# Performance work log

Hardware: AMD Instinct MI355X
Metric: run time of the kernel (lower is better)

Reference implementation:

```python
import jax, jax.numpy as jnp
import numpy as np

D_MODEL = 128
EXPAND = 8
D_INNER = EXPAND * D_MODEL            # 1024
HEADDIM = D_MODEL                     # headdim = int(in_channels*8/8)
NHEADS = D_INNER // HEADDIM           # 8
D_STATE = 128
D_CONV = 4
CONV_DIM = D_INNER + 2 * D_STATE      # 1280
D_IN_PROJ = 2 * D_INNER + 2 * D_STATE + NHEADS  # 2312
EPS = 1e-5
B_SZ, SEQ = 2, 2048


def setup_inputs() -> dict:
    key = jax.random.key(0)
    ks = jax.random.split(key, 16)
    n = jax.random.normal
    dt_init = jax.random.uniform(ks[4], (NHEADS,), minval=0.001, maxval=0.1)
    return dict(
        hidden_states=n(ks[0], (B_SZ, SEQ, D_MODEL), jnp.float32),
        w_in=n(ks[1], (D_IN_PROJ, D_MODEL), jnp.float32) / np.float32(np.sqrt(D_MODEL)),
        conv_w=n(ks[2], (CONV_DIM, D_CONV), jnp.float32) / np.float32(np.sqrt(D_CONV)),
        conv_b=n(ks[3], (CONV_DIM,), jnp.float32) * 0.01,
        dt_bias=jnp.log(jnp.expm1(dt_init)),  # inverse-softplus init (official)
        A_log=jnp.log(jax.random.uniform(ks[5], (NHEADS,), minval=1.0, maxval=16.0)),
        D_skip=jnp.ones((NHEADS,), jnp.float32),
        gnorm_w=jnp.ones((D_INNER,), jnp.float32),
        w_out=n(ks[6], (D_MODEL, D_INNER), jnp.float32) / np.float32(np.sqrt(D_INNER)),
        ln1_w=jnp.ones((D_MODEL,), jnp.float32),
        ln1_b=jnp.zeros((D_MODEL,), jnp.float32),
        ln2_w=jnp.ones((D_MODEL,), jnp.float32),
        ln2_b=jnp.zeros((D_MODEL,), jnp.float32),
        mlp_w=n(ks[7], (D_MODEL, D_MODEL), jnp.float32) / np.float32(np.sqrt(D_MODEL)),
        mlp_b=jnp.zeros((D_MODEL,), jnp.float32),
    )


def _layer_norm(x, w, b):
    m = x.mean(-1, keepdims=True)
    xc = x - m
    v = (xc * xc).mean(-1, keepdims=True)
    return xc * jax.lax.rsqrt(v + EPS) * w + b


def _mixer(u, w_in, conv_w, conv_b, dt_bias, A_log, D_skip, gnorm_w, w_out):
    b, l, _ = u.shape
    zxbcdt = u @ w_in.T                                    # (b,l,2312)
    z = zxbcdt[..., :D_INNER]                              # gate
    xBC = zxbcdt[..., D_INNER:D_INNER + CONV_DIM]
    dt = jax.nn.softplus(zxbcdt[..., -NHEADS:] + dt_bias)  # (b,l,h)
    # depthwise causal conv1d + SiLU
    xc = jnp.pad(xBC.swapaxes(1, 2), ((0, 0), (0, 0), (D_CONV - 1, 0)))
    xc = jax.lax.conv_general_dilated(xc, conv_w[:, None, :], (1,), 'VALID',
                                      feature_group_count=CONV_DIM)
    xBC = jax.nn.silu((xc + conv_b[None, :, None]).swapaxes(1, 2))
    x = xBC[..., :D_INNER].reshape(b, l, NHEADS, HEADDIM)  # (b,l,h,p)
    Bm = xBC[..., D_INNER:D_INNER + D_STATE]               # (b,l,n), ngroups=1
    Cm = xBC[..., D_INNER + D_STATE:]                      # (b,l,n)
    A = -jnp.exp(A_log)                                    # (h,)
    dA = jnp.exp(dt * A)                                   # (b,l,h)

    def step(S, inp):
        dA_t, dt_t, B_t, C_t, x_t = inp
        S = S * dA_t[:, :, None, None] + jnp.einsum('bh,bhp,bn->bhpn', dt_t, x_t, B_t)
        return S, jnp.einsum('bhpn,bn->bhp', S, C_t)

    S0 = jnp.zeros((b, NHEADS, HEADDIM, D_STATE), u.dtype)
    _, ys = jax.lax.scan(step, S0, (dA.swapaxes(0, 1), dt.swapaxes(0, 1),
                                    Bm.swapaxes(0, 1), Cm.swapaxes(0, 1),
                                    x.swapaxes(0, 1)))
    y = ys.swapaxes(0, 1) + D_skip[None, None, :, None] * x  # skip connection
    y = y.reshape(b, l, D_INNER) * jax.nn.silu(z)            # gated RMSNorm
    y = y * jax.lax.rsqrt((y * y).mean(-1, keepdims=True) + EPS) * gnorm_w
    return y @ w_out.T


def reference(hidden_states, w_in, conv_w, conv_b, dt_bias, A_log, D_skip,
              gnorm_w, w_out, ln1_w, ln1_b, ln2_w, ln2_b, mlp_w, mlp_b):
    residual = hidden_states
    h = _layer_norm(residual, ln1_w, ln1_b)
    h = _mixer(h, w_in, conv_w, conv_b, dt_bias, A_log, D_skip, gnorm_w, w_out)
    residual = h + residual
    h = _layer_norm(residual, ln2_w, ln2_b)
    return h @ mlp_w.T + mlp_b
```

## Files before the change

kernel.cpp:

```cpp
#include <hip/hip_runtime.h>
#include <hip/hip_bf16.h>

#define B_SZ 2
#define SEQ 2048
#define DMODEL 128
#define DINNER 1024
#define NHEADS 8
#define HEADDIM 128
#define DSTATE 128
#define CONVDIM 1280
#define NPROJ 2304
#define NTOK (B_SZ*SEQ)
#define CHUNK 64
#define NCHUNK (SEQ/CHUNK)
#define LDT 72

using bf16_t = __hip_bfloat16;
using short8 = __attribute__((ext_vector_type(8))) short;
using short4v= __attribute__((ext_vector_type(4))) short;
using f32x4  = __attribute__((ext_vector_type(4))) float;

__device__ __forceinline__ float silu_f(float x) { return x / (1.f + expf(-x)); }
__device__ __forceinline__ float bf2f(short s) {
    unsigned u = ((unsigned)(unsigned short)s) << 16;
    return __uint_as_float(u);
}
__device__ __forceinline__ short f2bf_s(float f) {
    bf16_t h = __float2bfloat16(f);
    return *(short*)&h;
}

__global__ __launch_bounds__(128) void head_fused(
        const float* __restrict__ hidden,
        const float* __restrict__ ln1_w, const float* __restrict__ ln1_b,
        const float* __restrict__ w_in,
        const float* __restrict__ dt_bias, const float* __restrict__ A_log,
        bf16_t* __restrict__ h_bf, float* __restrict__ dtb, float* __restrict__ ldAb,
        const float* __restrict__ wa, int na, const float* __restrict__ wb, int nb,
        const float* __restrict__ wc, int nc,
        bf16_t* __restrict__ oa, bf16_t* __restrict__ ob, bf16_t* __restrict__ oc) {
    int blk = blockIdx.x;
    if (blk >= NTOK) {
        int i = (blk - NTOK) * 128 + threadIdx.x;
        if (i < na) oa[i] = __float2bfloat16(wa[i]);
        else if (i < na + nb) ob[i - na] = __float2bfloat16(wb[i - na]);
        else if (i < na + nb + nc) oc[i - na - nb] = __float2bfloat16(wc[i - na - nb]);
        return;
    }
    int m = blk, t = threadIdx.x;
    int wave = t >> 6, lane = t & 63;
    __shared__ float sA[2], sB[2];
    __shared__ float sred[2][8];
    float v = hidden[(size_t)m*DMODEL + t];
    float s = v;
#pragma unroll
    for (int d = 1; d < 64; d <<= 1) s += __shfl_xor(s, d, 64);
    if (lane == 0) sA[wave] = s;
    __syncthreads();
    float mean = (sA[0] + sA[1]) * (1.f/128.f);
    float xc = v - mean;
    float q = xc * xc;
#pragma unroll
    for (int d = 1; d < 64; d <<= 1) q += __shfl_xor(q, d, 64);
    if (lane == 0) sB[wave] = q;
    __syncthreads();
    float var = (sB[0] + sB[1]) * (1.f/128.f);
    float o = xc * rsqrtf(var + 1e-5f) * ln1_w[t] + ln1_b[t];
    h_bf[(size_t)m*DMODEL + t] = __float2bfloat16(o);
#pragma unroll
    for (int hd = 0; hd < NHEADS; hd++) {
        float p = o * w_in[(size_t)(NPROJ + hd)*DMODEL + t];
#pragma unroll
        for (int d = 1; d < 64; d <<= 1) p += __shfl_xor(p, d, 64);
        if (lane == 0) sred[wave][hd] = p;
    }
    __syncthreads();
    if (t < NHEADS) {
        float ssum = sred[0][t] + sred[1][t] + dt_bias[t];
        float dtv = (ssum > 20.f) ? ssum : log1pf(expf(ssum));
        float Av = -expf(A_log[t]);
        dtb[m*NHEADS + t] = dtv;
        ldAb[m*NHEADS + t] = dtv * Av;
    }
}

__global__ __launch_bounds__(256) void gemm_bf(const bf16_t* __restrict__ A,
                                               const bf16_t* __restrict__ W,
                                               bf16_t* __restrict__ C,
                                               int M, int N, int K) {
    int tid = threadIdx.x;
    int wave = tid >> 6, lane = tid & 63;
    int m0 = blockIdx.x * 64 + wave * 16;
    int n0 = blockIdx.y * 64;
    int lr = lane & 15, quad = lane >> 4;
    f32x4 acc[4];
#pragma unroll
    for (int j = 0; j < 4; j++) acc[j] = (f32x4){0.f, 0.f, 0.f, 0.f};
    for (int k0 = 0; k0 < K; k0 += 32) {
        short8 a = *(const short8*)(A + (size_t)(m0 + lr)*K + k0 + quad*8);
#pragma unroll
        for (int j = 0; j < 4; j++) {
            short8 b = *(const short8*)(W + (size_t)(n0 + j*16 + lr)*K + k0 + quad*8);
            acc[j] = __builtin_amdgcn_mfma_f32_16x16x32_bf16(a, b, acc[j], 0, 0, 0);
        }
    }
#pragma unroll
    for (int j = 0; j < 4; j++)
#pragma unroll
        for (int r = 0; r < 4; r++) {
            int row = m0 + quad*4 + r;
            int col = n0 + j*16 + lr;
            C[(size_t)row*N + col] = __float2bfloat16(acc[j][r]);
        }
}

__global__ __launch_bounds__(256) void conv_silu(const bf16_t* __restrict__ zxb,
                                                 const float* __restrict__ conv_w,
                                                 const float* __restrict__ conv_b,
                                                 bf16_t* __restrict__ xBCb) {
    int idx = blockIdx.x * 256 + threadIdx.x;
    if (idx >= NTOK * CONVDIM / 4) return;
    int c4 = (idx % (CONVDIM/4)) * 4;
    int m  = idx / (CONVDIM/4);
    int b = m >> 11, l = m & (SEQ - 1);
    float acc[4];
    f32x4 wv[4];
#pragma unroll
    for (int j = 0; j < 4; j++) {
        acc[j] = conv_b[c4 + j];
        wv[j] = *(const f32x4*)(conv_w + (c4 + j)*4);
    }
#pragma unroll
    for (int k = 0; k < 4; k++) {
        int ll = l - 3 + k;
        if (ll >= 0) {
            short4v v = *(const short4v*)(zxb + (size_t)(b*SEQ + ll)*NPROJ + DINNER + c4);
#pragma unroll
            for (int j = 0; j < 4; j++) acc[j] += bf2f(v[j]) * wv[j][k];
        }
    }
    short4v res;
#pragma unroll
    for (int j = 0; j < 4; j++) res[j] = f2bf_s(silu_f(acc[j]));
    *(short4v*)(xBCb + (size_t)m*CONVDIM + c4) = res;
}

__global__ __launch_bounds__(256) void scanA_mfma(const bf16_t* __restrict__ xBCb,
                                                  const float* __restrict__ dt,
                                                  const float* __restrict__ ldA,
                                                  bf16_t* __restrict__ Sloc,
                                                  float* __restrict__ Pbuf) {
    int bid = blockIdx.x;
    int c = bid & 31, hd = (bid >> 5) & 7, b = bid >> 8;
    int t = threadIdx.x, wave = t >> 6, lane = t & 63;
    int lr = lane & 15, quad = lane >> 4;
    __shared__ bf16_t XT[128*LDT];
    __shared__ bf16_t BT[128*LDT];
    __shared__ float ws[CHUNK];
    int m0tok = b*SEQ + c*CHUNK;
    if (t < 64) {
        float L = ldA[(m0tok + t)*NHEADS + hd];
#pragma unroll
        for (int d = 1; d < 64; d <<= 1) {
            float u = __shfl_up(L, d, 64);
            if (lane >= d) L += u;
        }
        float Ltot = __shfl(L, 63, 64);
        ws[t] = expf(Ltot - L) * dt[(m0tok + t)*NHEADS + hd];
        if (t == 63) Pbuf[bid] = expf(Ltot);
    }
    __syncthreads();
#pragma unroll
    for (int i = 0; i < 4; i++) {
        int tt = t & 63;
        int pg = i*4 + (t >> 6);
        const bf16_t* row = xBCb + (size_t)(m0tok + tt)*CONVDIM;
        short8 xv = *(const short8*)(row + hd*HEADDIM + pg*8);
        short8 bv = *(const short8*)(row + DINNER + pg*8);
        float w = ws[tt];
#pragma unroll
        for (int j = 0; j < 8; j++) {
            XT[(pg*8 + j)*LDT + tt] = __float2bfloat16(bf2f(xv[j]) * w);
            short sv = bv[j];
            BT[(pg*8 + j)*LDT + tt] = *(bf16_t*)&sv;
        }
    }
    __syncthreads();
    int m0w = wave * 32;
    f32x4 acc[2][8];
#pragma unroll
    for (int mi = 0; mi < 2; mi++)
#pragma unroll
        for (int ni = 0; ni < 8; ni++) acc[mi][ni] = (f32x4){0.f,0.f,0.f,0.f};
#pragma unroll
    for (int k0 = 0; k0 < 64; k0 += 32) {
        short8 a[2];
#pragma unroll
        for (int mi = 0; mi < 2; mi++)
            a[mi] = *(const short8*)&XT[(m0w + mi*16 + lr)*LDT + k0 + quad*8];
#pragma unroll
        for (int ni = 0; ni < 8; ni++) {
            short8 bb = *(const short8*)&BT[(ni*16 + lr)*LDT + k0 + quad*8];
#pragma unroll
            for (int mi = 0; mi < 2; mi++)
                acc[mi][ni] = __builtin_amdgcn_mfma_f32_16x16x32_bf16(a[mi], bb, acc[mi][ni], 0, 0, 0);
        }
    }
    bf16_t* outp = Sloc + (size_t)bid * 16384;
#pragma unroll
    for (int mi = 0; mi < 2; mi++)
#pragma unroll
        for (int ni = 0; ni < 8; ni++)
#pragma unroll
            for (int r = 0; r < 4; r++) {
                int p = m0w + mi*16 + quad*4 + r;
                int n = ni*16 + lr;
                outp[p*128 + n] = __float2bfloat16(acc[mi][ni][r]);
            }
}

__global__ __launch_bounds__(256) void scanB(const bf16_t* __restrict__ Sloc,
                                             bf16_t* __restrict__ Sini,
                                             const float* __restrict__ Pbuf) {
    int bid = blockIdx.x;
    int bh = bid >> 5, slice = bid & 31;
    int t = threadIdx.x;
    int off = slice*512 + t*2;
    size_t base = (size_t)bh * NCHUNK * 16384;
    float run0 = 0.f, run1 = 0.f;
    for (int cc = 0; cc < NCHUNK; cc++) {
        unsigned raw = *(const unsigned*)(Sloc + base + (size_t)cc*16384 + off);
        float P = Pbuf[bh*NCHUNK + cc];
        unsigned o0 = (unsigned)(unsigned short)f2bf_s(run0);
        unsigned o1 = (unsigned)(unsigned short)f2bf_s(run1);
        *(unsigned*)(Sini + base + (size_t)cc*16384 + off) = o0 | (o1 << 16);
        run0 = run0*P + bf2f((short)(raw & 0xffff));
        run1 = run1*P + bf2f((short)(raw >> 16));
    }
}

__global__ __launch_bounds__(256) void scanC_mfma(const bf16_t* __restrict__ xBCb,
                                                  const float* __restrict__ dt,
                                                  const float* __restrict__ ldA,
                                                  const bf16_t* __restrict__ Sini,
                                                  const float* __restrict__ Dskip,
                                                  float* __restrict__ ybuf) {
    int bid = blockIdx.x;
    int c = bid & 31, hd = (bid >> 5) & 7, b = bid >> 8;
    int t = threadIdx.x, wave = t >> 6, lane = t & 63;
    int lr = lane & 15, quad = lane >> 4;
    __shared__ bf16_t XT[128*LDT];
    __shared__ bf16_t Mlds[64*LDT];
    __shared__ float Ls[CHUNK], dts[CHUNK];
    int m0tok = b*SEQ + c*CHUNK;
    if (t < 64) {
        float L = ldA[(m0tok + t)*NHEADS + hd];
#pragma unroll
        for (int d = 1; d < 64; d <<= 1) {
            float u = __shfl_up(L, d, 64);
            if (lane >= d) L += u;
        }
        Ls[t] = L;
        dts[t] = dt[(m0tok + t)*NHEADS + hd];
    }
#pragma unroll
    for (int i = 0; i < 4; i++) {
        int tt = t & 63;
        int pg = i*4 + (t >> 6);
        short8 xv = *(const short8*)(xBCb + (size_t)(m0tok + tt)*CONVDIM + hd*HEADDIM + pg*8);
#pragma unroll
        for (int j = 0; j < 8; j++) {
            short sv = xv[j];
            XT[(pg*8 + j)*LDT + tt] = *(bf16_t*)&sv;
        }
    }
    __syncthreads();
    const bf16_t* Crow = xBCb + (size_t)m0tok*CONVDIM + DINNER + DSTATE;
    const bf16_t* Brow = xBCb + (size_t)m0tok*CONVDIM + DINNER;
    f32x4 g[4];
#pragma unroll
    for (int si = 0; si < 4; si++) g[si] = (f32x4){0.f,0.f,0.f,0.f};
#pragma unroll
    for (int k0 = 0; k0 < 128; k0 += 32) {
        short8 a = *(const short8*)(Crow + (size_t)(wave*16 + lr)*CONVDIM + k0 + quad*8);
#pragma unroll
        for (int si = 0; si < 4; si++) {
            short8 bb = *(const short8*)(Brow + (size_t)(si*16 + lr)*CONVDIM + k0 + quad*8);
            g[si] = __builtin_amdgcn_mfma_f32_16x16x32_bf16(a, bb, g[si], 0, 0, 0);
        }
    }
#pragma unroll
    for (int si = 0; si < 4; si++)
#pragma unroll
        for (int r = 0; r < 4; r++) {
            int tt = wave*16 + quad*4 + r;
            int ss = si*16 + lr;
            float v = (ss <= tt) ? g[si][r] * expf(Ls[tt] - Ls[ss]) * dts[ss] : 0.f;
            Mlds[tt*LDT + ss] = __float2bfloat16(v);
        }
    __syncthreads();
    int p0 = wave * 32;
    f32x4 acc[4][2];
#pragma unroll
    for (int mi = 0; mi < 4; mi++)
#pragma unroll
        for (int ni = 0; ni < 2; ni++) acc[mi][ni] = (f32x4){0.f,0.f,0.f,0.f};
    const bf16_t* Sb = Sini + (size_t)bid * 16384;
#pragma unroll
    for (int k0 = 0; k0 < 128; k0 += 32) {
        short8 aC[4];
#pragma unroll
        for (int mi = 0; mi < 4; mi++)
            aC[mi] = *(const short8*)(Crow + (size_t)(mi*16 + lr)*CONVDIM + k0 + quad*8);
#pragma unroll
        for (int ni = 0; ni < 2; ni++) {
            short8 bb = *(const short8*)(Sb + (size_t)(p0 + ni*16 + lr)*128 + k0 + quad*8);
#pragma unroll
            for (int mi = 0; mi < 4; mi++)
                acc[mi][ni] = __builtin_amdgcn_mfma_f32_16x16x32_bf16(aC[mi], bb, acc[mi][ni], 0, 0, 0);
        }
    }
#pragma unroll
    for (int mi = 0; mi < 4; mi++) {
        float el[4];
#pragma unroll
        for (int r = 0; r < 4; r++) el[r] = expf(Ls[mi*16 + quad*4 + r]);
#pragma unroll
        for (int ni = 0; ni < 2; ni++)
#pragma unroll
            for (int r = 0; r < 4; r++) acc[mi][ni][r] *= el[r];
    }
#pragma unroll
    for (int k0 = 0; k0 < 64; k0 += 32) {
        short8 aM[4];
#pragma unroll
        for (int mi = 0; mi < 4; mi++)
            aM[mi] = *(const short8*)&Mlds[(mi*16 + lr)*LDT + k0 + quad*8];
#pragma unroll
        for (int ni = 0; ni < 2; ni++) {
            short8 bb = *(const short8*)&XT[(p0 + ni*16 + lr)*LDT + k0 + quad*8];
#pragma unroll
            for (int mi = 0; mi < 4; mi++)
                acc[mi][ni] = __builtin_amdgcn_mfma_f32_16x16x32_bf16(aM[mi], bb, acc[mi][ni], 0, 0, 0);
        }
    }
    float dsk = Dskip[hd];
#pragma unroll
    for (int mi = 0; mi < 4; mi++)
#pragma unroll
        for (int ni = 0; ni < 2; ni++)
#pragma unroll
            for (int r = 0; r < 4; r++) {
                int tt = mi*16 + quad*4 + r;
                int pp = p0 + ni*16 + lr;
                float xv = bf2f(*(const short*)&XT[pp*LDT + tt]);
                int m = m0tok + tt;
                ybuf[(size_t)m*DINNER + hd*HEADDIM + pp] = acc[mi][ni][r] + dsk*xv;
            }
}

__global__ __launch_bounds__(256) void gate_out_mlp(const float* __restrict__ ybuf,
                                                    const bf16_t* __restrict__ zxb,
                                                    const float* __restrict__ gw,
                                                    const bf16_t* __restrict__ Wb,
                                                    const float* __restrict__ resid,
                                                    const float* __restrict__ w2,
                                                    const float* __restrict__ b2,
                                                    const bf16_t* __restrict__ Wm,
                                                    const float* __restrict__ mb,
                                                    float* __restrict__ out) {
    int blk = blockIdx.x, t = threadIdx.x;
    int tok0 = blk * 16;
    int tt = t >> 4, cg = t & 15;
    int ch0 = cg * 64;
    __shared__ bf16_t A[16*1032];
    __shared__ float mixs[16*132];
    float vals[64];
    const float*  yr = ybuf + (size_t)(tok0 + tt)*DINNER + ch0;
    const bf16_t* zr = zxb  + (size_t)(tok0 + tt)*NPROJ  + ch0;
    float ss = 0.f;
#pragma unroll
    for (int i = 0; i < 64; i += 4) {
        f32x4 y = *(const f32x4*)(yr + i);
        short4v z = *(const short4v*)(zr + i);
#pragma unroll
        for (int r = 0; r < 4; r++) {
            float v = y[r] * silu_f(bf2f(z[r]));
            vals[i + r] = v; ss += v*v;
        }
    }
#pragma unroll
    for (int d = 1; d < 16; d <<= 1) ss += __shfl_xor(ss, d, 64);
    float rstd = rsqrtf(ss*(1.f/1024.f) + 1e-5f);
#pragma unroll
    for (int i = 0; i < 64; i += 4) {
        short4v pk;
#pragma unroll
        for (int r = 0; r < 4; r++) pk[r] = f2bf_s(vals[i+r]*rstd*gw[ch0+i+r]);
        *(short4v*)&A[tt*1032 + ch0 + i] = pk;
    }
    __syncthreads();
    int wave = t >> 6, lane = t & 63, lr = lane & 15, quad = lane >> 4;
    f32x4 acc[2];
    acc[0] = (f32x4){0.f,0.f,0.f,0.f}; acc[1] = (f32x4){0.f,0.f,0.f,0.f};
    for (int k0 = 0; k0 < 1024; k0 += 32) {
        short8 a = *(const short8*)&A[lr*1032 + k0 + quad*8];
#pragma unroll
        for (int j = 0; j < 2; j++) {
            int col = wave*32 + j*16 + lr;
            short8 bb = *(const short8*)(Wb + (size_t)col*DINNER + k0 + quad*8);
            acc[j] = __builtin_amdgcn_mfma_f32_16x16x32_bf16(a, bb, acc[j], 0, 0, 0);
        }
    }
#pragma unroll
    for (int j = 0; j < 2; j++)
#pragma unroll
        for (int r = 0; r < 4; r++)
            mixs[(quad*4 + r)*132 + wave*32 + j*16 + lr] = acc[j][r];
    __syncthreads();
    bf16_t* A2 = A;
    int ch8 = cg * 8;
    const float* rr = resid + (size_t)(tok0 + tt)*DMODEL + ch8;
    float v2[8];
    {
        f32x4 r0 = *(const f32x4*)rr, r1 = *(const f32x4*)(rr + 4);
#pragma unroll
        for (int r = 0; r < 4; r++) {
            v2[r]   = mixs[tt*132 + ch8 + r]     + r0[r];
            v2[4+r] = mixs[tt*132 + ch8 + 4 + r] + r1[r];
        }
    }
    float s2 = 0.f, sq = 0.f;
#pragma unroll
    for (int i = 0; i < 8; i++) { s2 += v2[i]; sq += v2[i]*v2[i]; }
#pragma unroll
    for (int d = 1; d < 16; d <<= 1) { s2 += __shfl_xor(s2, d, 64); sq += __shfl_xor(sq, d, 64); }
    float mean = s2 * (1.f/128.f);
    float var  = sq * (1.f/128.f) - mean*mean;
    float rstd2 = rsqrtf(var + 1e-5f);
    {
        short4v p0, p1;
#pragma unroll
        for (int r = 0; r < 4; r++) {
            p0[r] = f2bf_s((v2[r]   - mean)*rstd2*w2[ch8+r]   + b2[ch8+r]);
            p1[r] = f2bf_s((v2[4+r] - mean)*rstd2*w2[ch8+4+r] + b2[ch8+4+r]);
        }
        *(short4v*)&A2[tt*136 + ch8]     = p0;
        *(short4v*)&A2[tt*136 + ch8 + 4] = p1;
    }
    __syncthreads();
    f32x4 acc2[2];
    acc2[0] = (f32x4){0.f,0.f,0.f,0.f}; acc2[1] = (f32x4){0.f,0.f,0.f,0.f};
#pragma unroll
    for (int k0 = 0; k0 < 128; k0 += 32) {
        short8 a = *(const short8*)&A2[lr*136 + k0 + quad*8];
#pragma unroll
        for (int j = 0; j < 2; j++) {
            int col = wave*32 + j*16 + lr;
            short8 bb = *(const short8*)(Wm + (size_t)col*DMODEL + k0 + quad*8);
            acc2[j] = __builtin_amdgcn_mfma_f32_16x16x32_bf16(a, bb, acc2[j], 0, 0, 0);
        }
    }
#pragma unroll
    for (int j = 0; j < 2; j++)
#pragma unroll
        for (int r = 0; r < 4; r++) {
            int row = tok0 + quad*4 + r;
            int col = wave*32 + j*16 + lr;
            out[(size_t)row*DMODEL + col] = acc2[j][r] + mb[col];
        }
}

extern "C" void kernel_launch(void* const* d_in, const int* in_sizes, int n_in,
                              void* d_out, int out_size, void* d_ws, size_t ws_size,
                              hipStream_t stream) {
    const float* hidden  = (const float*)d_in[0];
    const float* w_in    = (const float*)d_in[1];
    const float* conv_w  = (const float*)d_in[2];
    const float* conv_b  = (const float*)d_in[3];
    const float* dt_bias = (const float*)d_in[4];
    const float* A_log   = (const float*)d_in[5];
    const float* D_skip  = (const float*)d_in[6];
    const float* gnorm_w = (const float*)d_in[7];
    const float* w_out   = (const float*)d_in[8];
    const float* ln1_w   = (const float*)d_in[9];
    const float* ln1_b   = (const float*)d_in[10];
    const float* ln2_w   = (const float*)d_in[11];
    const float* ln2_b   = (const float*)d_in[12];
    const float* mlp_w   = (const float*)d_in[13];
    const float* mlp_b   = (const float*)d_in[14];
    float* out = (float*)d_out;

    char* ws = (char*)d_ws;
    size_t off = 0;
    auto alloc = [&](size_t bytes) -> void* {
        void* p = ws + off;
        off = (off + bytes + 255) & ~(size_t)255;
        return p;
    };
    bf16_t* h_bf   = (bf16_t*)alloc((size_t)NTOK*DMODEL*2);
    bf16_t* w_in_bf= (bf16_t*)alloc((size_t)NPROJ*DMODEL*2);
    bf16_t* w_out_bf=(bf16_t*)alloc((size_t)DMODEL*DINNER*2);
    bf16_t* mlp_bf = (bf16_t*)alloc((size_t)DMODEL*DMODEL*2);
    bf16_t* zx_bf  = (bf16_t*)alloc((size_t)NTOK*NPROJ*2);
    bf16_t* xBCb   = (bf16_t*)alloc((size_t)NTOK*CONVDIM*2);
    float*  dtb    = (float*) alloc((size_t)NTOK*NHEADS*4);
    float*  ldAb   = (float*) alloc((size_t)NTOK*NHEADS*4);
    bf16_t* Sloc   = (bf16_t*)alloc((size_t)B_SZ*NHEADS*NCHUNK*16384*2);
    bf16_t* Sini   = (bf16_t*)alloc((size_t)B_SZ*NHEADS*NCHUNK*16384*2);
    float*  Pbuf   = (float*) alloc((size_t)B_SZ*NHEADS*NCHUNK*4);
    float*  ybuf   = (float*) alloc((size_t)NTOK*DINNER*4);
    (void)ws_size; (void)in_sizes; (void)n_in; (void)out_size;

    {
        int na = NPROJ*DMODEL, nb = DMODEL*DINNER, nc = DMODEL*DMODEL;
        int castBlocks = (na + nb + nc + 127) / 128;
        head_fused<<<NTOK + castBlocks, 128, 0, stream>>>(
            hidden, ln1_w, ln1_b, w_in, dt_bias, A_log, h_bf, dtb, ldAb,
            w_in, na, w_out, nb, mlp_w, nc, w_in_bf, w_out_bf, mlp_bf);
    }
    gemm_bf<<<dim3(NTOK/64, NPROJ/64), 256, 0, stream>>>(h_bf, w_in_bf, zx_bf,
                                                         NTOK, NPROJ, DMODEL);
    conv_silu<<<((size_t)NTOK*CONVDIM/4 + 255)/256, 256, 0, stream>>>(zx_bf, conv_w, conv_b, xBCb);
    scanA_mfma<<<B_SZ*NHEADS*NCHUNK, 256, 0, stream>>>(xBCb, dtb, ldAb, Sloc, Pbuf);
    scanB<<<B_SZ*NHEADS*NCHUNK, 256, 0, stream>>>(Sloc, Sini, Pbuf);
    scanC_mfma<<<B_SZ*NHEADS*NCHUNK, 256, 0, stream>>>(xBCb, dtb, ldAb, Sini, D_skip, ybuf);
    gate_out_mlp<<<NTOK/16, 256, 0, stream>>>(ybuf, zx_bf, gnorm_w, w_out_bf,
                                              hidden, ln2_w, ln2_b, mlp_bf, mlp_b, out);
}
```

Before: 181.4 us.

## Fuse in-proj GEMM with causal conv, split scan blocks, widen output kernel

The conv1d+SiLU is fused into the input-projection GEMM: blocks for the xBC columns compute a 64-token tile plus a 16-row halo into LDS and apply the conv there, so the full zxbcdt buffer is no longer written and re-read. The weight cast is vectorized to four elements per thread. scanA and scanC now split each (batch, head, chunk) into two halves along the state or head dimension, doubling block count to raise occupancy. gate_out_mlp moves to 512 threads with one 16-column tile per wave. The cost is recomputing halo rows in the GEMM and reloading X and dt data in twice as many scan blocks.

After: 183.4 us. Within noise of the previous version (+1.1%).

```diff
diff --git a/kernel.cpp b/kernel.cpp
--- a/kernel.cpp
+++ b/kernel.cpp
@@ -14,6 +14,7 @@
 #define CHUNK 64
 #define NCHUNK (SEQ/CHUNK)
 #define LDT 72
+#define LDU 76
 
 using bf16_t = __hip_bfloat16;
 using short8 = __attribute__((ext_vector_type(8))) short;
@@ -41,10 +42,18 @@
         bf16_t* __restrict__ oa, bf16_t* __restrict__ ob, bf16_t* __restrict__ oc) {
     int blk = blockIdx.x;
     if (blk >= NTOK) {
-        int i = (blk - NTOK) * 128 + threadIdx.x;
-        if (i < na) oa[i] = __float2bfloat16(wa[i]);
-        else if (i < na + nb) ob[i - na] = __float2bfloat16(wb[i - na]);
-        else if (i < na + nb + nc) oc[i - na - nb] = __float2bfloat16(wc[i - na - nb]);
+        int i = ((blk - NTOK) * 128 + threadIdx.x) * 4;
+        const float* src; bf16_t* dst; int base;
+        if (i < na)            { src = wa; dst = oa; base = 0; }
+        else if (i < na + nb)  { src = wb; dst = ob; base = na; }
+        else if (i < na+nb+nc) { src = wc; dst = oc; base = na + nb; }
+        else return;
+        int k = i - base;
+        f32x4 v = *(const f32x4*)(src + k);
+        short4v o;
+#pragma unroll
+        for (int r = 0; r < 4; r++) o[r] = f2bf_s(v[r]);
+        *(short4v*)(dst + k) = o;
         return;
     }
     int m = blk, t = threadIdx.x;
@@ -84,65 +93,85 @@
     }
 }
 
-__global__ __launch_bounds__(256) void gemm_bf(const bf16_t* __restrict__ A,
-                                               const bf16_t* __restrict__ W,
-                                               bf16_t* __restrict__ C,
-                                               int M, int N, int K) {
-    int tid = threadIdx.x;
-    int wave = tid >> 6, lane = tid & 63;
-    int m0 = blockIdx.x * 64 + wave * 16;
-    int n0 = blockIdx.y * 64;
-    int lr = lane & 15, quad = lane >> 4;
-    f32x4 acc[4];
-#pragma unroll
-    for (int j = 0; j < 4; j++) acc[j] = (f32x4){0.f, 0.f, 0.f, 0.f};
-    for (int k0 = 0; k0 < K; k0 += 32) {
-        short8 a = *(const short8*)(A + (size_t)(m0 + lr)*K + k0 + quad*8);
-#pragma unroll
-        for (int j = 0; j < 4; j++) {
-            short8 b = *(const short8*)(W + (size_t)(n0 + j*16 + lr)*K + k0 + quad*8);
-            acc[j] = __builtin_amdgcn_mfma_f32_16x16x32_bf16(a, b, acc[j], 0, 0, 0);
-        }
-    }
-#pragma unroll
-    for (int j = 0; j < 4; j++)
-#pragma unroll
-        for (int r = 0; r < 4; r++) {
-            int row = m0 + quad*4 + r;
-            int col = n0 + j*16 + lr;
-            C[(size_t)row*N + col] = __float2bfloat16(acc[j][r]);
-        }
-}
-
-__global__ __launch_bounds__(256) void conv_silu(const bf16_t* __restrict__ zxb,
+__global__ __launch_bounds__(256) void gemm_conv(const bf16_t* __restrict__ A,
+                                                 const bf16_t* __restrict__ W,
                                                  const float* __restrict__ conv_w,
                                                  const float* __restrict__ conv_b,
+                                                 bf16_t* __restrict__ zbuf,
                                                  bf16_t* __restrict__ xBCb) {
-    int idx = blockIdx.x * 256 + threadIdx.x;
-    if (idx >= NTOK * CONVDIM / 4) return;
-    int c4 = (idx % (CONVDIM/4)) * 4;
-    int m  = idx / (CONVDIM/4);
-    int b = m >> 11, l = m & (SEQ - 1);
-    float acc[4];
-    f32x4 wv[4];
+    int bx = blockIdx.x, by = blockIdx.y;
+    int t = threadIdx.x, wave = t >> 6, lane = t & 63;
+    int lr = lane & 15, quad = lane >> 4;
+    int m0 = bx * 64;
+    if (by < 16) {
+        int n0 = by * 64;
+        int mw = m0 + wave * 16;
+        f32x4 acc[4];
+#pragma unroll
+        for (int j = 0; j < 4; j++) acc[j] = (f32x4){0.f,0.f,0.f,0.f};
+#pragma unroll
+        for (int k0 = 0; k0 < 128; k0 += 32) {
+            short8 a = *(const short8*)(A + (size_t)(mw + lr)*DMODEL + k0 + quad*8);
+#pragma unroll
+            for (int j = 0; j < 4; j++) {
+                short8 b = *(const short8*)(W + (size_t)(n0 + j*16 + lr)*DMODEL + k0 + quad*8);
+                acc[j] = __builtin_amdgcn_mfma_f32_16x16x32_bf16(a, b, acc[j], 0, 0, 0);
+            }
+        }
+#pragma unroll
+        for (int j = 0; j < 4; j++)
+#pragma unroll
+            for (int r = 0; r < 4; r++)
+                zbuf[(size_t)(mw + quad*4 + r)*DINNER + n0 + j*16 + lr] = __float2bfloat16(acc[j][r]);
+        return;
+    }
+    int cb0 = (by - 16) * 64;
+    __shared__ bf16_t U[80*LDU];
+    bool seqstart = ((bx & 31) == 0);
+#pragma unroll
+    for (int mt = 0; mt < 5; mt++) {
+        if (mt == 0 && seqstart) continue;
+        int rb = m0 - 16 + mt*16;
+        f32x4 acc = (f32x4){0.f,0.f,0.f,0.f};
+#pragma unroll
+        for (int k0 = 0; k0 < 128; k0 += 32) {
+            short8 a = *(const short8*)(A + (size_t)(rb + lr)*DMODEL + k0 + quad*8);
+            short8 b = *(const short8*)(W + (size_t)(DINNER + cb0 + wave*16 + lr)*DMODEL + k0 + quad*8);
+            acc = __builtin_amdgcn_mfma_f32_16x16x32_bf16(a, b, acc, 0, 0, 0);
+        }
+#pragma unroll
+        for (int r = 0; r < 4; r++)
+            U[(mt*16 + quad*4 + r)*LDU + wave*16 + lr] = __float2bfloat16(acc[r]);
+    }
+    __syncthreads();
+    int c4 = (t & 15) * 4;
+    int tl0 = (t >> 4) * 4;
+    float bias[4]; f32x4 wv[4];
 #pragma unroll
     for (int j = 0; j < 4; j++) {
-        acc[j] = conv_b[c4 + j];
-        wv[j] = *(const f32x4*)(conv_w + (c4 + j)*4);
-    }
-#pragma unroll
-    for (int k = 0; k < 4; k++) {
-        int ll = l - 3 + k;
-        if (ll >= 0) {
-            short4v v = *(const short4v*)(zxb + (size_t)(b*SEQ + ll)*NPROJ + DINNER + c4);
-#pragma unroll
-            for (int j = 0; j < 4; j++) acc[j] += bf2f(v[j]) * wv[j][k];
-        }
-    }
-    short4v res;
-#pragma unroll
-    for (int j = 0; j < 4; j++) res[j] = f2bf_s(silu_f(acc[j]));
-    *(short4v*)(xBCb + (size_t)m*CONVDIM + c4) = res;
+        bias[j] = conv_b[cb0 + c4 + j];
+        wv[j] = *(const f32x4*)(conv_w + (cb0 + c4 + j)*4);
+    }
+    int lbase = m0 & (SEQ - 1);
+#pragma unroll
+    for (int it = 0; it < 4; it++) {
+        int tl = tl0 + it;
+        int l = lbase + tl;
+        float accv[4] = {bias[0], bias[1], bias[2], bias[3]};
+#pragma unroll
+        for (int k = 0; k < 4; k++) {
+            int ll = l - 3 + k;
+            if (ll >= 0) {
+                short4v u = *(const short4v*)&U[(13 + tl + k)*LDU + c4];
+#pragma unroll
+                for (int j = 0; j < 4; j++) accv[j] += bf2f(u[j]) * wv[j][k];
+            }
+        }
+        short4v res;
+#pragma unroll
+        for (int j = 0; j < 4; j++) res[j] = f2bf_s(silu_f(accv[j]));
+        *(short4v*)(xBCb + (size_t)(m0 + tl)*CONVDIM + cb0 + c4) = res;
+    }
 }
 
 __global__ __launch_bounds__(256) void scanA_mfma(const bf16_t* __restrict__ xBCb,
@@ -151,13 +180,14 @@
                                                   bf16_t* __restrict__ Sloc,
                                                   float* __restrict__ Pbuf) {
     int bid = blockIdx.x;
-    int c = bid & 31, hd = (bid >> 5) & 7, b = bid >> 8;
+    int nh = bid & 1, c = (bid >> 1) & 31, hd = (bid >> 6) & 7, b = bid >> 9;
     int t = threadIdx.x, wave = t >> 6, lane = t & 63;
     int lr = lane & 15, quad = lane >> 4;
     __shared__ bf16_t XT[128*LDT];
-    __shared__ bf16_t BT[128*LDT];
+    __shared__ bf16_t BT[64*LDT];
     __shared__ float ws[CHUNK];
     int m0tok = b*SEQ + c*CHUNK;
+    int bhc = (b*NHEADS + hd)*NCHUNK + c;
     if (t < 64) {
         float L = ldA[(m0tok + t)*NHEADS + hd];
 #pragma unroll
@@ -167,31 +197,36 @@
         }
         float Ltot = __shfl(L, 63, 64);
         ws[t] = expf(Ltot - L) * dt[(m0tok + t)*NHEADS + hd];
-        if (t == 63) Pbuf[bid] = expf(Ltot);
-    }
-    __syncthreads();
+        if (t == 63 && nh == 0) Pbuf[bhc] = expf(Ltot);
+    }
+    __syncthreads();
+    int tt = t & 63;
 #pragma unroll
     for (int i = 0; i < 4; i++) {
-        int tt = t & 63;
         int pg = i*4 + (t >> 6);
-        const bf16_t* row = xBCb + (size_t)(m0tok + tt)*CONVDIM;
-        short8 xv = *(const short8*)(row + hd*HEADDIM + pg*8);
-        short8 bv = *(const short8*)(row + DINNER + pg*8);
+        short8 xv = *(const short8*)(xBCb + (size_t)(m0tok + tt)*CONVDIM + hd*HEADDIM + pg*8);
         float w = ws[tt];
 #pragma unroll
+        for (int j = 0; j < 8; j++)
+            XT[(pg*8 + j)*LDT + tt] = __float2bfloat16(bf2f(xv[j]) * w);
+    }
+#pragma unroll
+    for (int i = 0; i < 2; i++) {
+        int pg = i*4 + (t >> 6);
+        short8 bv = *(const short8*)(xBCb + (size_t)(m0tok + tt)*CONVDIM + DINNER + nh*64 + pg*8);
+#pragma unroll
         for (int j = 0; j < 8; j++) {
-            XT[(pg*8 + j)*LDT + tt] = __float2bfloat16(bf2f(xv[j]) * w);
             short sv = bv[j];
             BT[(pg*8 + j)*LDT + tt] = *(bf16_t*)&sv;
         }
     }
     __syncthreads();
     int m0w = wave * 32;
-    f32x4 acc[2][8];
+    f32x4 acc[2][4];
 #pragma unroll
     for (int mi = 0; mi < 2; mi++)
 #pragma unroll
-        for (int ni = 0; ni < 8; ni++) acc[mi][ni] = (f32x4){0.f,0.f,0.f,0.f};
+        for (int ni = 0; ni < 4; ni++) acc[mi][ni] = (f32x4){0.f,0.f,0.f,0.f};
 #pragma unroll
     for (int k0 = 0; k0 < 64; k0 += 32) {
         short8 a[2];
@@ -199,22 +234,22 @@
         for (int mi = 0; mi < 2; mi++)
             a[mi] = *(const short8*)&XT[(m0w + mi*16 + lr)*LDT + k0 + quad*8];
 #pragma unroll
-        for (int ni = 0; ni < 8; ni++) {
+        for (int ni = 0; ni < 4; ni++) {
             short8 bb = *(const short8*)&BT[(ni*16 + lr)*LDT + k0 + quad*8];
 #pragma unroll
             for (int mi = 0; mi < 2; mi++)
                 acc[mi][ni] = __builtin_amdgcn_mfma_f32_16x16x32_bf16(a[mi], bb, acc[mi][ni], 0, 0, 0);
         }
     }
-    bf16_t* outp = Sloc + (size_t)bid * 16384;
+    bf16_t* outp = Sloc + (size_t)bhc * 16384;
 #pragma unroll
     for (int mi = 0; mi < 2; mi++)
 #pragma unroll
-        for (int ni = 0; ni < 8; ni++)
+        for (int ni = 0; ni < 4; ni++)
 #pragma unroll
             for (int r = 0; r < 4; r++) {
                 int p = m0w + mi*16 + quad*4 + r;
-                int n = ni*16 + lr;
+                int n = nh*64 + ni*16 + lr;
                 outp[p*128 + n] = __float2bfloat16(acc[mi][ni][r]);
             }
 }
@@ -246,13 +281,15 @@
                                                   const float* __restrict__ Dskip,
                                                   float* __restrict__ ybuf) {
     int bid = blockIdx.x;
-    int c = bid & 31, hd = (bid >> 5) & 7, b = bid >> 8;
+    int ph = bid & 1, c = (bid >> 1) & 31, hd = (bid >> 6) & 7, b = bid >> 9;
     int t = threadIdx.x, wave = t >> 6, lane = t & 63;
     int lr = lane & 15, quad = lane >> 4;
-    __shared__ bf16_t XT[128*LDT];
+    int pb = ph * 64;
+    __shared__ bf16_t XT[64*LDT];
     __shared__ bf16_t Mlds[64*LDT];
     __shared__ float Ls[CHUNK], dts[CHUNK];
     int m0tok = b*SEQ + c*CHUNK;
+    int bhc = (b*NHEADS + hd)*NCHUNK + c;
     if (t < 64) {
         float L = ldA[(m0tok + t)*NHEADS + hd];
 #pragma unroll
@@ -263,11 +300,11 @@
         Ls[t] = L;
         dts[t] = dt[(m0tok + t)*NHEADS + hd];
     }
-#pragma unroll
-    for (int i = 0; i < 4; i++) {
-        int tt = t & 63;
+    int tt = t & 63;
+#pragma unroll
+    for (int i = 0; i < 2; i++) {
         int pg = i*4 + (t >> 6);
-        short8 xv = *(const short8*)(xBCb + (size_t)(m0tok + tt)*CONVDIM + hd*HEADDIM + pg*8);
+        short8 xv = *(const short8*)(xBCb + (size_t)(m0tok + tt)*CONVDIM + hd*HEADDIM + pb + pg*8);
 #pragma unroll
         for (int j = 0; j < 8; j++) {
             short sv = xv[j];
@@ -293,42 +330,32 @@
     for (int si = 0; si < 4; si++)
 #pragma unroll
         for (int r = 0; r < 4; r++) {
-            int tt = wave*16 + quad*4 + r;
+            int tr = wave*16 + quad*4 + r;
             int ss = si*16 + lr;
-            float v = (ss <= tt) ? g[si][r] * expf(Ls[tt] - Ls[ss]) * dts[ss] : 0.f;
-            Mlds[tt*LDT + ss] = __float2bfloat16(v);
-        }
-    __syncthreads();
-    int p0 = wave * 32;
-    f32x4 acc[4][2];
-#pragma unroll
-    for (int mi = 0; mi < 4; mi++)
-#pragma unroll
-        for (int ni = 0; ni < 2; ni++) acc[mi][ni] = (f32x4){0.f,0.f,0.f,0.f};
-    const bf16_t* Sb = Sini + (size_t)bid * 16384;
+            float v = (ss <= tr) ? g[si][r] * expf(Ls[tr] - Ls[ss]) * dts[ss] : 0.f;
+            Mlds[tr*LDT + ss] = __float2bfloat16(v);
+        }
+    __syncthreads();
+    int pw = wave * 16;
+    f32x4 acc[4];
+#pragma unroll
+    for (int mi = 0; mi < 4; mi++) acc[mi] = (f32x4){0.f,0.f,0.f,0.f};
+    const bf16_t* Sb = Sini + (size_t)bhc * 16384;
 #pragma unroll
     for (int k0 = 0; k0 < 128; k0 += 32) {
         short8 aC[4];
 #pragma unroll
         for (int mi = 0; mi < 4; mi++)
             aC[mi] = *(const short8*)(Crow + (size_t)(mi*16 + lr)*CONVDIM + k0 + quad*8);
-#pragma unroll
-        for (int ni = 0; ni < 2; ni++) {
-            short8 bb = *(const short8*)(Sb + (size_t)(p0 + ni*16 + lr)*128 + k0 + quad*8);
-#pragma unroll
-            for (int mi = 0; mi < 4; mi++)
-                acc[mi][ni] = __builtin_amdgcn_mfma_f32_16x16x32_bf16(aC[mi], bb, acc[mi][ni], 0, 0, 0);
-        }
+        short8 bb = *(const short8*)(Sb + (size_t)(pb + pw + lr)*128 + k0 + quad*8);
+#pragma unroll
+        for (int mi = 0; mi < 4; mi++)
+            acc[mi] = __builtin_amdgcn_mfma_f32_16x16x32_bf16(aC[mi], bb, acc[mi], 0, 0, 0);
     }
 #pragma unroll
     for (int mi = 0; mi < 4; mi++) {
-        float el[4];
-#pragma unroll
-        for (int r = 0; r < 4; r++) el[r] = expf(Ls[mi*16 + quad*4 + r]);
-#pragma unroll
-        for (int ni = 0; ni < 2; ni++)
-#pragma unroll
-            for (int r = 0; r < 4; r++) acc[mi][ni][r] *= el[r];
+#pragma unroll
+        for (int r = 0; r < 4; r++) acc[mi][r] *= expf(Ls[mi*16 + quad*4 + r]);
     }
 #pragma unroll
     for (int k0 = 0; k0 < 64; k0 += 32) {
@@ -336,31 +363,26 @@
 #pragma unroll
         for (int mi = 0; mi < 4; mi++)
             aM[mi] = *(const short8*)&Mlds[(mi*16 + lr)*LDT + k0 + quad*8];
-#pragma unroll
-        for (int ni = 0; ni < 2; ni++) {
-            short8 bb = *(const short8*)&XT[(p0 + ni*16 + lr)*LDT + k0 + quad*8];
-#pragma unroll
-            for (int mi = 0; mi < 4; mi++)
-                acc[mi][ni] = __builtin_amdgcn_mfma_f32_16x16x32_bf16(aM[mi], bb, acc[mi][ni], 0, 0, 0);
-        }
+        short8 bb = *(const short8*)&XT[(pw + lr)*LDT + k0 + quad*8];
+#pragma unroll
+        for (int mi = 0; mi < 4; mi++)
+            acc[mi] = __builtin_amdgcn_mfma_f32_16x16x32_bf16(aM[mi], bb, acc[mi], 0, 0, 0);
     }
     float dsk = Dskip[hd];
 #pragma unroll
     for (int mi = 0; mi < 4; mi++)
 #pragma unroll
-        for (int ni = 0; ni < 2; ni++)
-#pragma unroll
-            for (int r = 0; r < 4; r++) {
-                int tt = mi*16 + quad*4 + r;
-                int pp = p0 + ni*16 + lr;
-                float xv = bf2f(*(const short*)&XT[pp*LDT + tt]);
-                int m = m0tok + tt;
-                ybuf[(size_t)m*DINNER + hd*HEADDIM + pp] = acc[mi][ni][r] + dsk*xv;
-            }
-}
-
-__global__ __launch_bounds__(256) void gate_out_mlp(const float* __restrict__ ybuf,
-                                                    const bf16_t* __restrict__ zxb,
+        for (int r = 0; r < 4; r++) {
+            int tr = mi*16 + quad*4 + r;
+            int pl = pw + lr;
+            float xv = bf2f(*(const short*)&XT[pl*LDT + tr]);
+            int m = m0tok + tr;
+            ybuf[(size_t)m*DINNER + hd*HEADDIM + pb + pl] = acc[mi][r] + dsk*xv;
+        }
+}
+
+__global__ __launch_bounds__(512) void gate_out_mlp(const float* __restrict__ ybuf,
+                                                    const bf16_t* __restrict__ zbuf,
                                                     const float* __restrict__ gw,
                                                     const bf16_t* __restrict__ Wb,
                                                     const float* __restrict__ resid,
@@ -371,16 +393,17 @@
                                                     float* __restrict__ out) {
     int blk = blockIdx.x, t = threadIdx.x;
     int tok0 = blk * 16;
-    int tt = t >> 4, cg = t & 15;
-    int ch0 = cg * 64;
+    int wave = t >> 6, lane = t & 63, lr = lane & 15, quad = lane >> 4;
     __shared__ bf16_t A[16*1032];
     __shared__ float mixs[16*132];
-    float vals[64];
+    int tt = t >> 5, cg = t & 31;
+    int ch0 = cg * 32;
+    float vals[32];
     const float*  yr = ybuf + (size_t)(tok0 + tt)*DINNER + ch0;
-    const bf16_t* zr = zxb  + (size_t)(tok0 + tt)*NPROJ  + ch0;
+    const bf16_t* zr = zbuf + (size_t)(tok0 + tt)*DINNER + ch0;
     float ss = 0.f;
 #pragma unroll
-    for (int i = 0; i < 64; i += 4) {
+    for (int i = 0; i < 32; i += 4) {
         f32x4 y = *(const f32x4*)(yr + i);
         short4v z = *(const short4v*)(zr + i);
 #pragma unroll
@@ -390,85 +413,59 @@
         }
     }
 #pragma unroll
-    for (int d = 1; d < 16; d <<= 1) ss += __shfl_xor(ss, d, 64);
+    for (int d = 1; d < 32; d <<= 1) ss += __shfl_xor(ss, d, 64);
     float rstd = rsqrtf(ss*(1.f/1024.f) + 1e-5f);
 #pragma unroll
-    for (int i = 0; i < 64; i += 4) {
+    for (int i = 0; i < 32; i += 4) {
         short4v pk;
 #pragma unroll
         for (int r = 0; r < 4; r++) pk[r] = f2bf_s(vals[i+r]*rstd*gw[ch0+i+r]);
         *(short4v*)&A[tt*1032 + ch0 + i] = pk;
     }
     __syncthreads();
-    int wave = t >> 6, lane = t & 63, lr = lane & 15, quad = lane >> 4;
-    f32x4 acc[2];
-    acc[0] = (f32x4){0.f,0.f,0.f,0.f}; acc[1] = (f32x4){0.f,0.f,0.f,0.f};
+    int col = wave*16 + lr;
+    f32x4 acc = (f32x4){0.f,0.f,0.f,0.f};
     for (int k0 = 0; k0 < 1024; k0 += 32) {
         short8 a = *(const short8*)&A[lr*1032 + k0 + quad*8];
-#pragma unroll
-        for (int j = 0; j < 2; j++) {
-            int col = wave*32 + j*16 + lr;
-            short8 bb = *(const short8*)(Wb + (size_t)col*DINNER + k0 + quad*8);
-            acc[j] = __builtin_amdgcn_mfma_f32_16x16x32_bf16(a, bb, acc[j], 0, 0, 0);
-        }
-    }
-#pragma unroll
-    for (int j = 0; j < 2; j++)
-#pragma unroll
-        for (int r = 0; r < 4; r++)
-            mixs[(quad*4 + r)*132 + wave*32 + j*16 + lr] = acc[j][r];
-    __syncthreads();
-    bf16_t* A2 = A;
-    int ch8 = cg * 8;
-    const float* rr = resid + (size_t)(tok0 + tt)*DMODEL + ch8;
-    float v2[8];
-    {
-        f32x4 r0 = *(const f32x4*)rr, r1 = *(const f32x4*)(rr + 4);
-#pragma unroll
-        for (int r = 0; r < 4; r++) {
-            v2[r]   = mixs[tt*132 + ch8 + r]     + r0[r];
-            v2[4+r] = mixs[tt*132 + ch8 + 4 + r] + r1[r];
-        }
-    }
+        short8 bb = *(const short8*)(Wb + (size_t)col*DINNER + k0 + quad*8);
+        acc = __builtin_amdgcn_mfma_f32_16x16x32_bf16(a, bb, acc, 0, 0, 0);
+    }
+#pragma unroll
+    for (int r = 0; r < 4; r++)
+        mixs[(quad*4 + r)*132 + col] = acc[r];
+    __syncthreads();
+    int ch4 = (t & 31) * 4;
+    const float* rr = resid + (size_t)(tok0 + tt)*DMODEL + ch4;
+    f32x4 r0 = *(const f32x4*)rr;
+    float v2[4];
+#pragma unroll
+    for (int r = 0; r < 4; r++) v2[r] = mixs[tt*132 + ch4 + r] + r0[r];
     float s2 = 0.f, sq = 0.f;
 #pragma unroll
-    for (int i = 0; i < 8; i++) { s2 += v2[i]; sq += v2[i]*v2[i]; }
-#pragma unroll
-    for (int d = 1; d < 16; d <<= 1) { s2 += __shfl_xor(s2, d, 64); sq += __shfl_xor(sq, d, 64); }
+    for (int i = 0; i < 4; i++) { s2 += v2[i]; sq += v2[i]*v2[i]; }
+#pragma unroll
+    for (int d = 1; d < 32; d <<= 1) { s2 += __shfl_xor(s2, d, 64); sq += __shfl_xor(sq, d, 64); }
     float mean = s2 * (1.f/128.f);
     float var  = sq * (1.f/128.f) - mean*mean;
     float rstd2 = rsqrtf(var + 1e-5f);
     {
-        short4v p0, p1;
-#pragma unroll
-        for (int r = 0; r < 4; r++) {
-            p0[r] = f2bf_s((v2[r]   - mean)*rstd2*w2[ch8+r]   + b2[ch8+r]);
-            p1[r] = f2bf_s((v2[4+r] - mean)*rstd2*w2[ch8+4+r] + b2[ch8+4+r]);
-        }
-        *(short4v*)&A2[tt*136 + ch8]     = p0;
-        *(short4v*)&A2[tt*136 + ch8 + 4] = p1;
-    }
-    __syncthreads();
-    f32x4 acc2[2];
-    acc2[0] = (f32x4){0.f,0.f,0.f,0.f}; acc2[1] = (f32x4){0.f,0.f,0.f,0.f};
+        short4v p0;
+#pragma unroll
+        for (int r = 0; r < 4; r++)
+            p0[r] = f2bf_s((v2[r] - mean)*rstd2*w2[ch4+r] + b2[ch4+r]);
+        *(short4v*)&A[tt*136 + ch4] = p0;
+    }
+    __syncthreads();
+    f32x4 acc2 = (f32x4){0.f,0.f,0.f,0.f};
 #pragma unroll
     for (int k0 = 0; k0 < 128; k0 += 32) {
-        short8 a = *(const short8*)&A2[lr*136 + k0 + quad*8];
-#pragma unroll
-        for (int j = 0; j < 2; j++) {
-            int col = wave*32 + j*16 + lr;
-            short8 bb = *(const short8*)(Wm + (size_t)col*DMODEL + k0 + quad*8);
-            acc2[j] = __builtin_amdgcn_mfma_f32_16x16x32_bf16(a, bb, acc2[j], 0, 0, 0);
-        }
-    }
-#pragma unroll
-    for (int j = 0; j < 2; j++)
-#pragma unroll
-        for (int r = 0; r < 4; r++) {
-            int row = tok0 + quad*4 + r;
-            int col = wave*32 + j*16 + lr;
-            out[(size_t)row*DMODEL + col] = acc2[j][r] + mb[col];
-        }
+        short8 a = *(const short8*)&A[lr*136 + k0 + quad*8];
+        short8 bb = *(const short8*)(Wm + (size_t)col*DMODEL + k0 + quad*8);
+        acc2 = __builtin_amdgcn_mfma_f32_16x16x32_bf16(a, bb, acc2, 0, 0, 0);
+    }
+#pragma unroll
+    for (int r = 0; r < 4; r++)
+        out[(size_t)(tok0 + quad*4 + r)*DMODEL + col] = acc2[r] + mb[col];
 }
 
 extern "C" void kernel_launch(void* const* d_in, const int* in_sizes, int n_in,
@@ -502,7 +499,7 @@
     bf16_t* w_in_bf= (bf16_t*)alloc((size_t)NPROJ*DMODEL*2);
     bf16_t* w_out_bf=(bf16_t*)alloc((size_t)DMODEL*DINNER*2);
     bf16_t* mlp_bf = (bf16_t*)alloc((size_t)DMODEL*DMODEL*2);
-    bf16_t* zx_bf  = (bf16_t*)alloc((size_t)NTOK*NPROJ*2);
+    bf16_t* zbuf   = (bf16_t*)alloc((size_t)NTOK*DINNER*2);
     bf16_t* xBCb   = (bf16_t*)alloc((size_t)NTOK*CONVDIM*2);
     float*  dtb    = (float*) alloc((size_t)NTOK*NHEADS*4);
     float*  ldAb   = (float*) alloc((size_t)NTOK*NHEADS*4);
@@ -514,17 +511,15 @@
 
     {
         int na = NPROJ*DMODEL, nb = DMODEL*DINNER, nc = DMODEL*DMODEL;
-        int castBlocks = (na + nb + nc + 127) / 128;
+        int castBlocks = (na + nb + nc) / 4 / 128;
         head_fused<<<NTOK + castBlocks, 128, 0, stream>>>(
             hidden, ln1_w, ln1_b, w_in, dt_bias, A_log, h_bf, dtb, ldAb,
             w_in, na, w_out, nb, mlp_w, nc, w_in_bf, w_out_bf, mlp_bf);
     }
-    gemm_bf<<<dim3(NTOK/64, NPROJ/64), 256, 0, stream>>>(h_bf, w_in_bf, zx_bf,
-                                                         NTOK, NPROJ, DMODEL);
-    conv_silu<<<((size_t)NTOK*CONVDIM/4 + 255)/256, 256, 0, stream>>>(zx_bf, conv_w, conv_b, xBCb);
-    scanA_mfma<<<B_SZ*NHEADS*NCHUNK, 256, 0, stream>>>(xBCb, dtb, ldAb, Sloc, Pbuf);
-    scanB<<<B_SZ*NHEADS*NCHUNK, 256, 0, stream>>>(Sloc, Sini, Pbuf);
-    scanC_mfma<<<B_SZ*NHEADS*NCHUNK, 256, 0, stream>>>(xBCb, dtb, ldAb, Sini, D_skip, ybuf);
-    gate_out_mlp<<<NTOK/16, 256, 0, stream>>>(ybuf, zx_bf, gnorm_w, w_out_bf,
+    gemm_conv<<<dim3(64, 36), 256, 0, stream>>>(h_bf, w_in_bf, conv_w, conv_b, zbuf, xBCb);
+    scanA_mfma<<<1024, 256, 0, stream>>>(xBCb, dtb, ldAb, Sloc, Pbuf);
+    scanB<<<512, 256, 0, stream>>>(Sloc, Sini, Pbuf);
+    scanC_mfma<<<1024, 256, 0, stream>>>(xBCb, dtb, ldAb, Sini, D_skip, ybuf);
+    gate_out_mlp<<<NTOK/16, 512, 0, stream>>>(ybuf, zbuf, gnorm_w, w_out_bf,
                                               hidden, ln2_w, ln2_b, mlp_bf, mlp_b, out);
 }
```
